# Performance work log

Measured on AMD Instinct MI355X. Metric: run time of the kernel, lower is better.

The kernel has to match this reference:

```python
import jax, jax.numpy as jnp
import numpy as np

N_NODES = 50000
N_EDGES = 1600000
IN_CH, HID_CH, OUT_CH = 512, 128, 64


def gcn_conv(x, edge_index, edge_weight, W, b, n_nodes):
    """PyG GCNConv: add self-loops (weight 1), symmetric normalization,
    out = scatter_add(norm * (xW)[src] -> dst) + b."""
    src, dst = edge_index[0], edge_index[1]
    loop = jnp.arange(n_nodes, dtype=edge_index.dtype)
    src_f = jnp.concatenate([src, loop])
    dst_f = jnp.concatenate([dst, loop])
    ew_f = jnp.concatenate([edge_weight, jnp.ones((n_nodes,), edge_weight.dtype)])
    # degree over target nodes (includes self-loop weight)
    deg = jax.ops.segment_sum(ew_f, dst_f, num_segments=n_nodes)
    dinv = jnp.where(deg > 0, jax.lax.rsqrt(deg), 0.0)
    norm = dinv[src_f] * ew_f * dinv[dst_f]  # [E+N]
    h = x @ W                                 # [N, out] dense GEMM first (cheaper gather)
    msg = h[src_f] * norm[:, None]            # [E+N, out] gather + scale
    out = jax.ops.segment_sum(msg, dst_f, num_segments=n_nodes)
    return out + b


def setup_inputs() -> dict:
    key = jax.random.key(0)
    ks = jax.random.split(key, 10)
    x = jax.random.normal(ks[0], (N_NODES, IN_CH), dtype=jnp.float32)
    edge_index = jax.random.randint(ks[1], (2, N_EDGES), 0, N_NODES, dtype=jnp.int32)
    edge_weight = jax.random.uniform(ks[2], (N_EDGES,), dtype=jnp.float32)
    def glorot(k, fan_in, fan_out):
        s = (6.0 / (fan_in + fan_out)) ** 0.5
        return jax.random.uniform(k, (fan_in, fan_out), jnp.float32, -s, s)
    W1 = glorot(ks[3], IN_CH, HID_CH)
    b1 = jnp.zeros((HID_CH,), jnp.float32)
    W2 = glorot(ks[4], HID_CH, OUT_CH)
    b2 = jnp.zeros((OUT_CH,), jnp.float32)
    W3 = glorot(ks[5], HID_CH, OUT_CH)
    b3 = jnp.zeros((OUT_CH,), jnp.float32)
    return {"x": x, "edge_index": edge_index, "edge_weight": edge_weight,
            "W1": W1, "b1": b1, "W2": W2, "b2": b2, "W3": W3, "b3": b3}


def reference(x, edge_index, edge_weight, W1, b1, W2, b2, W3, b3):
    n = x.shape[0]
    h = jax.nn.relu(gcn_conv(x, edge_index, edge_weight, W1, b1, n))
    mean = gcn_conv(h, edge_index, edge_weight, W2, b2, n)
    logstd = gcn_conv(h, edge_index, edge_weight, W3, b3, n)
    return (mean, logstd)
```

## Files before the change

kernel.cpp:

```cpp
#include <hip/hip_runtime.h>


#define THREADS 256
#define SCAN_CHUNK 2048
#define D 4

#define DEG_MASK ((1ULL << 40) - 1)
#define CNT_SHIFT 40

typedef __attribute__((ext_vector_type(8))) short short8;
typedef __attribute__((ext_vector_type(4))) float floatx4;

__device__ __forceinline__ unsigned short f32_to_bf16(float v) {
    return (unsigned short)((__float_as_uint(v) + 0x8000u) >> 16);
}

__global__ __launch_bounds__(THREADS) void zero_kernel(float* __restrict__ p, int n) {
    int i = blockIdx.x * THREADS + threadIdx.x;
    if (i < n) p[i] = 0.0f;
}

__global__ __launch_bounds__(THREADS) void deg_count_kernel(
    const int* __restrict__ ei, const float* __restrict__ ew,
    unsigned long long* __restrict__ deg_cnt, int* __restrict__ rank, int E) {
    int e = blockIdx.x * THREADS + threadIdx.x;
    if (e >= E) return;
    int d = ei[E + e];
    float w = ew[e];
    unsigned long long q = (unsigned long long)(w * 4294967296.0f);
    unsigned long long old = atomicAdd(&deg_cnt[d], (1ULL << CNT_SHIFT) | q);
    rank[e] = (int)(old >> CNT_SHIFT);
}

__global__ __launch_bounds__(THREADS) void scan_part1(
    const unsigned long long* __restrict__ deg_cnt,
    float* __restrict__ dinvv, int* __restrict__ partials, int n) {
    int t = threadIdx.x;
    int base = blockIdx.x * SCAN_CHUNK + t * 8;
    int s = 0;
#pragma unroll
    for (int i = 0; i < 8; ++i) {
        int idx = base + i;
        if (idx < n) {
            unsigned long long v = deg_cnt[idx];
            s += (int)(v >> CNT_SHIFT);
            float dg = (float)(v & DEG_MASK) * 0x1p-32f;
            dinvv[idx] = rsqrtf(dg + 1.0f);
        }
    }
    __shared__ int sm[THREADS];
    sm[t] = s;
    __syncthreads();
    for (int off = THREADS / 2; off > 0; off >>= 1) {
        if (t < off) sm[t] += sm[t + off];
        __syncthreads();
    }
    if (t == 0) partials[blockIdx.x] = sm[0];
}

__global__ __launch_bounds__(1024) void scan_part2(int* __restrict__ partials, int nb) {
    __shared__ int s[1024];
    int t = threadIdx.x;
    int v = (t < nb) ? partials[t] : 0;
    s[t] = v;
    __syncthreads();
    for (int off = 1; off < 1024; off <<= 1) {
        int x = (t >= off) ? s[t - off] : 0;
        __syncthreads();
        s[t] += x;
        __syncthreads();
    }
    if (t < nb) partials[t] = s[t] - v;
}

__global__ __launch_bounds__(THREADS) void scan_part3(
    const unsigned long long* __restrict__ deg_cnt, const int* __restrict__ partials,
    int* __restrict__ offs, int n) {
    int t = threadIdx.x;
    int base = blockIdx.x * SCAN_CHUNK + t * 8;
    int loc[8];
    int s = 0;
#pragma unroll
    for (int i = 0; i < 8; ++i) {
        int idx = base + i;
        int c = (idx < n) ? (int)(deg_cnt[idx] >> CNT_SHIFT) : 0;
        loc[i] = c;
        s += c;
    }
    __shared__ int sm[THREADS];
    sm[t] = s;
    __syncthreads();
    for (int off = 1; off < THREADS; off <<= 1) {
        int x = (t >= off) ? sm[t - off] : 0;
        __syncthreads();
        sm[t] += x;
        __syncthreads();
    }
    int run = partials[blockIdx.x] + sm[t] - s;
#pragma unroll
    for (int i = 0; i < 8; ++i) {
        int idx = base + i;
        if (idx < n) {
            offs[idx] = run;
            run += loc[i];
            if (idx == n - 1) offs[n] = run;
        }
    }
}

__global__ __launch_bounds__(THREADS) void fill_kernel(
    const int* __restrict__ ei, const float* __restrict__ ew,
    const float* __restrict__ dinvv, const int* __restrict__ offs,
    const int* __restrict__ rank, int2* __restrict__ csr, int E) {
    int e = blockIdx.x * THREADS + threadIdx.x;
    if (e >= E) return;
    int s = ei[e], d = ei[E + e];
    int pos = offs[d] + rank[e];
    csr[pos] = make_int2(s, __float_as_int(dinvv[s] * ew[e] * dinvv[d]));
}

__global__ __launch_bounds__(THREADS) void wsplit_kernel(
    const float* __restrict__ W, unsigned short* __restrict__ hi,
    unsigned short* __restrict__ lo) {
    int id = blockIdx.x * THREADS + threadIdx.x;
    if (id >= 512 * 128) return;
    int k = id >> 7, n = id & 127;
    float v = W[id];
    unsigned int b = __float_as_uint(v);
    unsigned short h = (unsigned short)(b >> 16);
    float fh = __uint_as_float(b & 0xFFFF0000u);
    unsigned short l = (unsigned short)(__float_as_uint(v - fh) >> 16);
    hi[n * 512 + k] = h;
    lo[n * 512 + k] = l;
}

__global__ __launch_bounds__(THREADS) void gemm1_mfma_kernel(
    const float* __restrict__ A, const unsigned short* __restrict__ Wth,
    const unsigned short* __restrict__ Wtl, unsigned short* __restrict__ C, int M) {
    __shared__ unsigned short As[2][64][72];
    __shared__ unsigned short Bs[2][128][72];
    int t = threadIdx.x;
    int brow0 = blockIdx.x * 64;
    int arow = t >> 2, akq = (t & 3) * 16;
    int bn = t >> 1, bkoff = (t & 1) * 32;
    int wid = t >> 6, lane = t & 63;
    int wr = wid >> 1, wc = wid & 1;
    int lm = lane & 15, lk = (lane >> 4) * 8;
    floatx4 acc[2][4];
#pragma unroll
    for (int i = 0; i < 2; i++)
#pragma unroll
        for (int j = 0; j < 4; j++) acc[i][j] = (floatx4)0.0f;

    int gr = brow0 + arow;
    for (int k0 = 0; k0 < 512; k0 += 64) {
        __syncthreads();
        {
            const float* ap = &A[(size_t)gr * 512 + k0 + akq];
#pragma unroll
            for (int i = 0; i < 4; ++i) {
                float4 v = (gr < M) ? *(const float4*)&ap[i * 4]
                                    : make_float4(0.f, 0.f, 0.f, 0.f);
                float e[4] = {v.x, v.y, v.z, v.w};
                ushort4 h4, l4;
                unsigned short* hp = (unsigned short*)&h4;
                unsigned short* lp = (unsigned short*)&l4;
#pragma unroll
                for (int c = 0; c < 4; ++c) {
                    unsigned int b = __float_as_uint(e[c]);
                    hp[c] = (unsigned short)(b >> 16);
                    float fh = __uint_as_float(b & 0xFFFF0000u);
                    lp[c] = (unsigned short)(__float_as_uint(e[c] - fh) >> 16);
                }
                *(ushort4*)&As[0][arow][akq + i * 4] = h4;
                *(ushort4*)&As[1][arow][akq + i * 4] = l4;
            }
        }
        {
            const unsigned short* bh = &Wth[(size_t)bn * 512 + k0 + bkoff];
            const unsigned short* bl = &Wtl[(size_t)bn * 512 + k0 + bkoff];
#pragma unroll
            for (int s = 0; s < 4; ++s) {
                *(float4*)&Bs[0][bn][bkoff + s * 8] = *(const float4*)&bh[s * 8];
                *(float4*)&Bs[1][bn][bkoff + s * 8] = *(const float4*)&bl[s * 8];
            }
        }
        __syncthreads();
#pragma unroll
        for (int kc = 0; kc < 2; ++kc) {
            int kb = kc * 32 + lk;
            short8 ah[2], al[2], bh[4], bl[4];
#pragma unroll
            for (int mf = 0; mf < 2; ++mf) {
                ah[mf] = *(const short8*)&As[0][wr * 32 + mf * 16 + lm][kb];
                al[mf] = *(const short8*)&As[1][wr * 32 + mf * 16 + lm][kb];
            }
#pragma unroll
            for (int nf = 0; nf < 4; ++nf) {
                bh[nf] = *(const short8*)&Bs[0][wc * 64 + nf * 16 + lm][kb];
                bl[nf] = *(const short8*)&Bs[1][wc * 64 + nf * 16 + lm][kb];
            }
#pragma unroll
            for (int mf = 0; mf < 2; ++mf)
#pragma unroll
                for (int nf = 0; nf < 4; ++nf) {
                    acc[mf][nf] = __builtin_amdgcn_mfma_f32_16x16x32_bf16(
                        ah[mf], bh[nf], acc[mf][nf], 0, 0, 0);
                    acc[mf][nf] = __builtin_amdgcn_mfma_f32_16x16x32_bf16(
                        ah[mf], bl[nf], acc[mf][nf], 0, 0, 0);
                    acc[mf][nf] = __builtin_amdgcn_mfma_f32_16x16x32_bf16(
                        al[mf], bh[nf], acc[mf][nf], 0, 0, 0);
                }
        }
    }
#pragma unroll
    for (int mf = 0; mf < 2; ++mf) {
        int rbase = brow0 + wr * 32 + mf * 16 + (lane >> 4) * 4;
#pragma unroll
        for (int nf = 0; nf < 4; ++nf) {
            int col = wc * 64 + nf * 16 + lm;
#pragma unroll
            for (int r = 0; r < 4; ++r) {
                int g = rbase + r;
                if (g < M) C[(size_t)g * 128 + col] = f32_to_bf16(acc[mf][nf][r]);
            }
        }
    }
}

__global__ __launch_bounds__(THREADS) void spmm_bf16_kernel(
    const unsigned short* __restrict__ feat, const float* __restrict__ dinvv,
    const int* __restrict__ offs, const int2* __restrict__ csr,
    const float* __restrict__ bias, unsigned short* __restrict__ outb,
    float* __restrict__ outf, int n, int do_relu) {
    int gw = (blockIdx.x * THREADS + threadIdx.x) >> 6;
    int lane = threadIdx.x & 63;
    if (gw >= n) return;
    const int d = __builtin_amdgcn_readfirstlane(gw);
    float di = dinvv[d];
    float sw = di * di;
    const unsigned int* __restrict__ f1 = (const unsigned int*)feat + lane;
    unsigned int sv = f1[(size_t)d * 64];
    float2 acc;
    acc.x = __uint_as_float(sv << 16) * sw;
    acc.y = __uint_as_float(sv & 0xFFFF0000u) * sw;
    int j0 = offs[d];
    int m = offs[d + 1] - j0;
    const int2* __restrict__ cp = csr + j0;

    int2 eA[D], eB[D];
    float wA[D], wB[D];
    unsigned int vA[D], vB[D];

#pragma unroll
    for (int i = 0; i < D; ++i) if (i < m) eA[i] = cp[i];
#pragma unroll
    for (int i = 0; i < D; ++i) if (D + i < m) eB[i] = cp[D + i];
#pragma unroll
    for (int i = 0; i < D; ++i) if (i < m) {
        wA[i] = __int_as_float(eA[i].y);
        vA[i] = f1[(size_t)eA[i].x * 64];
    }

    int g = 0;
    for (; g + 4 * D <= m; g += 2 * D) {
#pragma unroll
        for (int i = 0; i < D; ++i) eA[i] = cp[g + 2 * D + i];
#pragma unroll
        for (int i = 0; i < D; ++i) {
            wB[i] = __int_as_float(eB[i].y);
            vB[i] = f1[(size_t)eB[i].x * 64];
        }
#pragma unroll
        for (int i = 0; i < D; ++i) {
            acc.x = fmaf(wA[i], __uint_as_float(vA[i] << 16), acc.x);
            acc.y = fmaf(wA[i], __uint_as_float(vA[i] & 0xFFFF0000u), acc.y);
        }
#pragma unroll
        for (int i = 0; i < D; ++i) eB[i] = cp[g + 3 * D + i];
#pragma unroll
        for (int i = 0; i < D; ++i) {
            wA[i] = __int_as_float(eA[i].y);
            vA[i] = f1[(size_t)eA[i].x * 64];
        }
#pragma unroll
        for (int i = 0; i < D; ++i) {
            acc.x = fmaf(wB[i], __uint_as_float(vB[i] << 16), acc.x);
            acc.y = fmaf(wB[i], __uint_as_float(vB[i] & 0xFFFF0000u), acc.y);
        }
    }
#pragma unroll
    for (int i = 0; i < D; ++i) if (g + i < m) {
        acc.x = fmaf(wA[i], __uint_as_float(vA[i] << 16), acc.x);
        acc.y = fmaf(wA[i], __uint_as_float(vA[i] & 0xFFFF0000u), acc.y);
    }
    g += D;
#pragma unroll
    for (int i = 0; i < D; ++i) if (g + i < m) {
        float w = __int_as_float(eB[i].y);
        unsigned int v = f1[(size_t)eB[i].x * 64];
        acc.x = fmaf(w, __uint_as_float(v << 16), acc.x);
        acc.y = fmaf(w, __uint_as_float(v & 0xFFFF0000u), acc.y);
    }
    g += D;
    for (; g < m; ++g) {
        int2 e = cp[g];
        float w = __int_as_float(e.y);
        unsigned int v = f1[(size_t)e.x * 64];
        acc.x = fmaf(w, __uint_as_float(v << 16), acc.x);
        acc.y = fmaf(w, __uint_as_float(v & 0xFFFF0000u), acc.y);
    }

    if (bias) {
        float2 b = *(const float2*)&bias[lane * 2];
        acc.x += b.x;
        acc.y += b.y;
    }
    if (do_relu) {
        acc.x = fmaxf(acc.x, 0.0f);
        acc.y = fmaxf(acc.y, 0.0f);
    }
    if (outb) {
        unsigned int lo = (__float_as_uint(acc.x) + 0x8000u) >> 16;
        unsigned int hi = (__float_as_uint(acc.y) + 0x8000u) & 0xFFFF0000u;
        ((unsigned int*)outb)[(size_t)d * 64 + lane] = hi | lo;
    } else {
        ((float2*)outf)[(size_t)d * 64 + lane] = acc;
    }
}

__global__ __launch_bounds__(THREADS) void gemm23_kernel(
    const float* __restrict__ A, const float* __restrict__ W2,
    const float* __restrict__ W3, const float* __restrict__ b2,
    const float* __restrict__ b3, float* __restrict__ outm,
    float* __restrict__ outl, int M) {
    __shared__ float As[16][68];
    __shared__ float Bs[16][128];
    int t = threadIdx.x;
    int ty = t >> 4, tx = t & 15;
    int brow0 = blockIdx.x * 64;
    int arow = t >> 2, aq = t & 3;
    int bkr = t >> 5, bcol = (t & 31) * 4;
    float acc[4][8];
#pragma unroll
    for (int i = 0; i < 4; i++)
#pragma unroll
        for (int j = 0; j < 8; j++) acc[i][j] = 0.0f;
    int gr = brow0 + arow;
    const float4 z4 = make_float4(0.f, 0.f, 0.f, 0.f);
    for (int k0 = 0; k0 < 128; k0 += 16) {
        float4 av = (gr < M) ? *(const float4*)&A[(size_t)gr * 128 + k0 + aq * 4] : z4;
        int k1 = k0 + bkr, k2 = k0 + bkr + 8;
        float4 b0 = (bcol < 64) ? *(const float4*)&W2[(size_t)k1 * 64 + bcol]
                                : *(const float4*)&W3[(size_t)k1 * 64 + bcol - 64];
        float4 b1 = (bcol < 64) ? *(const float4*)&W2[(size_t)k2 * 64 + bcol]
                                : *(const float4*)&W3[(size_t)k2 * 64 + bcol - 64];
        __syncthreads();
        As[aq * 4 + 0][arow] = av.x;
        As[aq * 4 + 1][arow] = av.y;
        As[aq * 4 + 2][arow] = av.z;
        As[aq * 4 + 3][arow] = av.w;
        *(float4*)&Bs[bkr][bcol] = b0;
        *(float4*)&Bs[bkr + 8][bcol] = b1;
        __syncthreads();
#pragma unroll
        for (int kk = 0; kk < 16; ++kk) {
            float4 a = *(const float4*)&As[kk][ty * 4];
            float4 p0 = *(const float4*)&Bs[kk][tx * 8];
            float4 p1 = *(const float4*)&Bs[kk][tx * 8 + 4];
            float av_[4] = {a.x, a.y, a.z, a.w};
            float bv_[8] = {p0.x, p0.y, p0.z, p0.w, p1.x, p1.y, p1.z, p1.w};
#pragma unroll
            for (int i = 0; i < 4; i++)
#pragma unroll
                for (int j = 0; j < 8; j++)
                    acc[i][j] = fmaf(av_[i], bv_[j], acc[i][j]);
        }
    }
    bool is_mean = (tx < 8);
    int c = is_mean ? tx * 8 : tx * 8 - 64;
    const float* bb = is_mean ? b2 : b3;
    float* op = is_mean ? outm : outl;
    float4 bias0 = *(const float4*)&bb[c];
    float4 bias1 = *(const float4*)&bb[c + 4];
#pragma unroll
    for (int i = 0; i < 4; i++) {
        int r = brow0 + ty * 4 + i;
        if (r < M) {
            *(float4*)&op[(size_t)r * 64 + c] =
                make_float4(acc[i][0] + bias0.x, acc[i][1] + bias0.y,
                            acc[i][2] + bias0.z, acc[i][3] + bias0.w);
            *(float4*)&op[(size_t)r * 64 + c + 4] =
                make_float4(acc[i][4] + bias1.x, acc[i][5] + bias1.y,
                            acc[i][6] + bias1.z, acc[i][7] + bias1.w);
        }
    }
}

extern "C" void kernel_launch(void* const* d_in, const int* in_sizes, int n_in,
                              void* d_out, int out_size, void* d_ws, size_t ws_size,
                              hipStream_t stream) {
    const float* x  = (const float*)d_in[0];
    const int*   ei = (const int*)d_in[1];
    const float* ew = (const float*)d_in[2];
    const float* W1 = (const float*)d_in[3];
    const float* b1 = (const float*)d_in[4];
    const float* W2 = (const float*)d_in[5];
    const float* b2 = (const float*)d_in[6];
    const float* W3 = (const float*)d_in[7];
    const float* b3 = (const float*)d_in[8];

    const int n = in_sizes[0] / 512;
    const int E = in_sizes[2];
    const int nb_scan = (n + SCAN_CHUNK - 1) / SCAN_CHUNK;

    char* p = (char*)d_ws;
    auto alloc = [&](size_t bytes) {
        char* q = p;
        p += (bytes + 511) & ~(size_t)511;
        return q;
    };
    unsigned long long* deg_cnt = (unsigned long long*)alloc((size_t)n * 8);
    float* dinvv  = (float*)alloc((size_t)n * 4);
    int*   offs   = (int*)alloc((size_t)(n + 1) * 4);
    int*   rank   = (int*)alloc((size_t)E * 4);
    int*   partials = (int*)alloc((size_t)nb_scan * 4);
    int2*  csr    = (int2*)alloc((size_t)E * 8);
    unsigned short* Wth = (unsigned short*)alloc((size_t)512 * 128 * 2);
    unsigned short* Wtl = (unsigned short*)alloc((size_t)512 * 128 * 2);
    unsigned short* h0b = (unsigned short*)alloc((size_t)n * 128 * 2);
    unsigned short* hbb = (unsigned short*)alloc((size_t)n * 128 * 2);
    float* agg2   = (float*)alloc((size_t)n * 128 * 4);

    float* outm = (float*)d_out;
    float* outl = outm + (size_t)n * 64;

    zero_kernel<<<(2 * n + THREADS - 1) / THREADS, THREADS, 0, stream>>>((float*)deg_cnt, 2 * n);
    deg_count_kernel<<<(E + THREADS - 1) / THREADS, THREADS, 0, stream>>>(ei, ew, deg_cnt, rank, E);
    scan_part1<<<nb_scan, THREADS, 0, stream>>>(deg_cnt, dinvv, partials, n);
    scan_part2<<<1, 1024, 0, stream>>>(partials, nb_scan);
    scan_part3<<<nb_scan, THREADS, 0, stream>>>(deg_cnt, partials, offs, n);
    fill_kernel<<<(E + THREADS - 1) / THREADS, THREADS, 0, stream>>>(ei, ew, dinvv, offs,
                                                                     rank, csr, E);
    wsplit_kernel<<<(512 * 128 + THREADS - 1) / THREADS, THREADS, 0, stream>>>(W1, Wth, Wtl);
    gemm1_mfma_kernel<<<(n + 63) / 64, THREADS, 0, stream>>>(x, Wth, Wtl, h0b, n);
    spmm_bf16_kernel<<<((size_t)n * 64 + THREADS - 1) / THREADS, THREADS, 0, stream>>>(
        h0b, dinvv, offs, csr, b1, hbb, nullptr, n, 1);
    spmm_bf16_kernel<<<((size_t)n * 64 + THREADS - 1) / THREADS, THREADS, 0, stream>>>(
        hbb, dinvv, offs, csr, nullptr, nullptr, agg2, n, 0);
    gemm23_kernel<<<(n + 63) / 64, THREADS, 0, stream>>>(agg2, W2, W3, b2, b3, outm, outl, n);
}
```

Measured before the change: 481.3 us.

## Interleave degree-count atomics with GEMM1 blocks in one fused launch

Merges the degree/rank atomic counting kernel into the first GEMM kernel. Blocks are split by role: one in every nine runs a GEMM tile and the other eight do edge atomics. The aim is to overlap the latency-bound atomic scatter with the compute-bound MFMA GEMM and to drop one launch. The cost is that the atomic-role blocks carry the GEMM kernel's shared-memory footprint, which may reduce occupancy, and block scheduling becomes less predictable.

```diff
diff --git a/kernel.cpp b/kernel.cpp
--- a/kernel.cpp
+++ b/kernel.cpp
@@ -4,6 +4,7 @@
 #define THREADS 256
 #define SCAN_CHUNK 2048
 #define D 4
+#define ILV 9
 
 #define DEG_MASK ((1ULL << 40) - 1)
 #define CNT_SHIFT 40
@@ -18,105 +19,6 @@
 __global__ __launch_bounds__(THREADS) void zero_kernel(float* __restrict__ p, int n) {
     int i = blockIdx.x * THREADS + threadIdx.x;
     if (i < n) p[i] = 0.0f;
-}
-
-__global__ __launch_bounds__(THREADS) void deg_count_kernel(
-    const int* __restrict__ ei, const float* __restrict__ ew,
-    unsigned long long* __restrict__ deg_cnt, int* __restrict__ rank, int E) {
-    int e = blockIdx.x * THREADS + threadIdx.x;
-    if (e >= E) return;
-    int d = ei[E + e];
-    float w = ew[e];
-    unsigned long long q = (unsigned long long)(w * 4294967296.0f);
-    unsigned long long old = atomicAdd(&deg_cnt[d], (1ULL << CNT_SHIFT) | q);
-    rank[e] = (int)(old >> CNT_SHIFT);
-}
-
-__global__ __launch_bounds__(THREADS) void scan_part1(
-    const unsigned long long* __restrict__ deg_cnt,
-    float* __restrict__ dinvv, int* __restrict__ partials, int n) {
-    int t = threadIdx.x;
-    int base = blockIdx.x * SCAN_CHUNK + t * 8;
-    int s = 0;
-#pragma unroll
-    for (int i = 0; i < 8; ++i) {
-        int idx = base + i;
-        if (idx < n) {
-            unsigned long long v = deg_cnt[idx];
-            s += (int)(v >> CNT_SHIFT);
-            float dg = (float)(v & DEG_MASK) * 0x1p-32f;
-            dinvv[idx] = rsqrtf(dg + 1.0f);
-        }
-    }
-    __shared__ int sm[THREADS];
-    sm[t] = s;
-    __syncthreads();
-    for (int off = THREADS / 2; off > 0; off >>= 1) {
-        if (t < off) sm[t] += sm[t + off];
-        __syncthreads();
-    }
-    if (t == 0) partials[blockIdx.x] = sm[0];
-}
-
-__global__ __launch_bounds__(1024) void scan_part2(int* __restrict__ partials, int nb) {
-    __shared__ int s[1024];
-    int t = threadIdx.x;
-    int v = (t < nb) ? partials[t] : 0;
-    s[t] = v;
-    __syncthreads();
-    for (int off = 1; off < 1024; off <<= 1) {
-        int x = (t >= off) ? s[t - off] : 0;
-        __syncthreads();
-        s[t] += x;
-        __syncthreads();
-    }
-    if (t < nb) partials[t] = s[t] - v;
-}
-
-__global__ __launch_bounds__(THREADS) void scan_part3(
-    const unsigned long long* __restrict__ deg_cnt, const int* __restrict__ partials,
-    int* __restrict__ offs, int n) {
-    int t = threadIdx.x;
-    int base = blockIdx.x * SCAN_CHUNK + t * 8;
-    int loc[8];
-    int s = 0;
-#pragma unroll
-    for (int i = 0; i < 8; ++i) {
-        int idx = base + i;
-        int c = (idx < n) ? (int)(deg_cnt[idx] >> CNT_SHIFT) : 0;
-        loc[i] = c;
-        s += c;
-    }
-    __shared__ int sm[THREADS];
-    sm[t] = s;
-    __syncthreads();
-    for (int off = 1; off < THREADS; off <<= 1) {
-        int x = (t >= off) ? sm[t - off] : 0;
-        __syncthreads();
-        sm[t] += x;
-        __syncthreads();
-    }
-    int run = partials[blockIdx.x] + sm[t] - s;
-#pragma unroll
-    for (int i = 0; i < 8; ++i) {
-        int idx = base + i;
-        if (idx < n) {
-            offs[idx] = run;
-            run += loc[i];
-            if (idx == n - 1) offs[n] = run;
-        }
-    }
-}
-
-__global__ __launch_bounds__(THREADS) void fill_kernel(
-    const int* __restrict__ ei, const float* __restrict__ ew,
-    const float* __restrict__ dinvv, const int* __restrict__ offs,
-    const int* __restrict__ rank, int2* __restrict__ csr, int E) {
-    int e = blockIdx.x * THREADS + threadIdx.x;
-    if (e >= E) return;
-    int s = ei[e], d = ei[E + e];
-    int pos = offs[d] + rank[e];
-    csr[pos] = make_int2(s, __float_as_int(dinvv[s] * ew[e] * dinvv[d]));
 }
 
 __global__ __launch_bounds__(THREADS) void wsplit_kernel(
@@ -134,13 +36,33 @@
     lo[n * 512 + k] = l;
 }
 
-__global__ __launch_bounds__(THREADS) void gemm1_mfma_kernel(
+__global__ __launch_bounds__(THREADS) void fused_gemm1_deg_kernel(
     const float* __restrict__ A, const unsigned short* __restrict__ Wth,
-    const unsigned short* __restrict__ Wtl, unsigned short* __restrict__ C, int M) {
+    const unsigned short* __restrict__ Wtl, unsigned short* __restrict__ C, int M,
+    const int* __restrict__ ei, const float* __restrict__ ew,
+    unsigned long long* __restrict__ deg_cnt, int* __restrict__ rank, int E,
+    int gemm_blocks) {
     __shared__ unsigned short As[2][64][72];
     __shared__ unsigned short Bs[2][128][72];
+    int bid = blockIdx.x;
+    int role = bid % ILV;
     int t = threadIdx.x;
-    int brow0 = blockIdx.x * 64;
+
+    if (role != 0) {
+        int db = (bid / ILV) * (ILV - 1) + (role - 1);
+        int e = db * THREADS + t;
+        if (e >= E) return;
+        int d = ei[E + e];
+        float w = ew[e];
+        unsigned long long q = (unsigned long long)(w * 4294967296.0f);
+        unsigned long long old = atomicAdd(&deg_cnt[d], (1ULL << CNT_SHIFT) | q);
+        rank[e] = (int)(old >> CNT_SHIFT);
+        return;
+    }
+
+    int gb = bid / ILV;
+    if (gb >= gemm_blocks) return;
+    int brow0 = gb * 64;
     int arow = t >> 2, akq = (t & 3) * 16;
     int bn = t >> 1, bkoff = (t & 1) * 32;
     int wid = t >> 6, lane = t & 63;
@@ -161,16 +83,16 @@
             for (int i = 0; i < 4; ++i) {
                 float4 v = (gr < M) ? *(const float4*)&ap[i * 4]
                                     : make_float4(0.f, 0.f, 0.f, 0.f);
-                float e[4] = {v.x, v.y, v.z, v.w};
+                float e4[4] = {v.x, v.y, v.z, v.w};
                 ushort4 h4, l4;
                 unsigned short* hp = (unsigned short*)&h4;
                 unsigned short* lp = (unsigned short*)&l4;
 #pragma unroll
                 for (int c = 0; c < 4; ++c) {
-                    unsigned int b = __float_as_uint(e[c]);
+                    unsigned int b = __float_as_uint(e4[c]);
                     hp[c] = (unsigned short)(b >> 16);
                     float fh = __uint_as_float(b & 0xFFFF0000u);
-                    lp[c] = (unsigned short)(__float_as_uint(e[c] - fh) >> 16);
+                    lp[c] = (unsigned short)(__float_as_uint(e4[c] - fh) >> 16);
                 }
                 *(ushort4*)&As[0][arow][akq + i * 4] = h4;
                 *(ushort4*)&As[1][arow][akq + i * 4] = l4;
@@ -226,6 +148,93 @@
             }
         }
     }
+}
+
+__global__ __launch_bounds__(THREADS) void scan_part1(
+    const unsigned long long* __restrict__ deg_cnt,
+    float* __restrict__ dinvv, int* __restrict__ partials, int n) {
+    int t = threadIdx.x;
+    int base = blockIdx.x * SCAN_CHUNK + t * 8;
+    int s = 0;
+#pragma unroll
+    for (int i = 0; i < 8; ++i) {
+        int idx = base + i;
+        if (idx < n) {
+            unsigned long long v = deg_cnt[idx];
+            s += (int)(v >> CNT_SHIFT);
+            float dg = (float)(v & DEG_MASK) * 0x1p-32f;
+            dinvv[idx] = rsqrtf(dg + 1.0f);
+        }
+    }
+    __shared__ int sm[THREADS];
+    sm[t] = s;
+    __syncthreads();
+    for (int off = THREADS / 2; off > 0; off >>= 1) {
+        if (t < off) sm[t] += sm[t + off];
+        __syncthreads();
+    }
+    if (t == 0) partials[blockIdx.x] = sm[0];
+}
+
+__global__ __launch_bounds__(1024) void scan_part2(int* __restrict__ partials, int nb) {
+    __shared__ int s[1024];
+    int t = threadIdx.x;
+    int v = (t < nb) ? partials[t] : 0;
+    s[t] = v;
+    __syncthreads();
+    for (int off = 1; off < 1024; off <<= 1) {
+        int x = (t >= off) ? s[t - off] : 0;
+        __syncthreads();
+        s[t] += x;
+        __syncthreads();
+    }
+    if (t < nb) partials[t] = s[t] - v;
+}
+
+__global__ __launch_bounds__(THREADS) void scan_part3(
+    const unsigned long long* __restrict__ deg_cnt, const int* __restrict__ partials,
+    int* __restrict__ offs, int n) {
+    int t = threadIdx.x;
+    int base = blockIdx.x * SCAN_CHUNK + t * 8;
+    int loc[8];
+    int s = 0;
+#pragma unroll
+    for (int i = 0; i < 8; ++i) {
+        int idx = base + i;
+        int c = (idx < n) ? (int)(deg_cnt[idx] >> CNT_SHIFT) : 0;
+        loc[i] = c;
+        s += c;
+    }
+    __shared__ int sm[THREADS];
+    sm[t] = s;
+    __syncthreads();
+    for (int off = 1; off < THREADS; off <<= 1) {
+        int x = (t >= off) ? sm[t - off] : 0;
+        __syncthreads();
+        sm[t] += x;
+        __syncthreads();
+    }
+    int run = partials[blockIdx.x] + sm[t] - s;
+#pragma unroll
+    for (int i = 0; i < 8; ++i) {
+        int idx = base + i;
+        if (idx < n) {
+            offs[idx] = run;
+            run += loc[i];
+            if (idx == n - 1) offs[n] = run;
+        }
+    }
+}
+
+__global__ __launch_bounds__(THREADS) void fill_kernel(
+    const int* __restrict__ ei, const float* __restrict__ ew,
+    const float* __restrict__ dinvv, const int* __restrict__ offs,
+    const int* __restrict__ rank, int2* __restrict__ csr, int E) {
+    int e = blockIdx.x * THREADS + threadIdx.x;
+    if (e >= E) return;
+    int s = ei[e], d = ei[E + e];
+    int pos = offs[d] + rank[e];
+    csr[pos] = make_int2(s, __float_as_int(dinvv[s] * ew[e] * dinvv[d]));
 }
 
 __global__ __launch_bounds__(THREADS) void spmm_bf16_kernel(
@@ -435,15 +444,24 @@
     float* outm = (float*)d_out;
     float* outl = outm + (size_t)n * 64;
 
+    const int gemm_blocks = (n + 63) / 64;
+    const int deg_blocks  = (E + THREADS - 1) / THREADS;
+    int fused_grid = gemm_blocks * ILV;
+    {
+        int need = (deg_blocks + (ILV - 1) - 1) / (ILV - 1);
+        int alt = need * ILV;
+        if (alt > fused_grid) fused_grid = alt;
+    }
+
     zero_kernel<<<(2 * n + THREADS - 1) / THREADS, THREADS, 0, stream>>>((float*)deg_cnt, 2 * n);
-    deg_count_kernel<<<(E + THREADS - 1) / THREADS, THREADS, 0, stream>>>(ei, ew, deg_cnt, rank, E);
+    wsplit_kernel<<<(512 * 128 + THREADS - 1) / THREADS, THREADS, 0, stream>>>(W1, Wth, Wtl);
+    fused_gemm1_deg_kernel<<<fused_grid, THREADS, 0, stream>>>(
+        x, Wth, Wtl, h0b, n, ei, ew, deg_cnt, rank, E, gemm_blocks);
     scan_part1<<<nb_scan, THREADS, 0, stream>>>(deg_cnt, dinvv, partials, n);
     scan_part2<<<1, 1024, 0, stream>>>(partials, nb_scan);
     scan_part3<<<nb_scan, THREADS, 0, stream>>>(deg_cnt, partials, offs, n);
     fill_kernel<<<(E + THREADS - 1) / THREADS, THREADS, 0, stream>>>(ei, ew, dinvv, offs,
                                                                      rank, csr, E);
-    wsplit_kernel<<<(512 * 128 + THREADS - 1) / THREADS, THREADS, 0, stream>>>(W1, Wth, Wtl);
-    gemm1_mfma_kernel<<<(n + 63) / 64, THREADS, 0, stream>>>(x, Wth, Wtl, h0b, n);
     spmm_bf16_kernel<<<((size_t)n * 64 + THREADS - 1) / THREADS, THREADS, 0, stream>>>(
         h0b, dinvv, offs, csr, b1, hbb, nullptr, n, 1);
     spmm_bf16_kernel<<<((size_t)n * 64 + THREADS - 1) / THREADS, THREADS, 0, stream>>>(
```

New measurement: 445.1 us. 7.5% less time.
